# Kernel optimization log

Hardware: AMD Instinct MI355X
Metric: run time of the kernel (lower is better)

Reference implementation:

```python
import jax, jax.numpy as jnp
import numpy as np

NUM_HEADS = 6

def setup_inputs() -> dict:
    key = jax.random.key(0)
    ks = jax.random.split(key, 6)
    B_, N, C = 4096, 64, 192
    nW = 4096
    return {
        "x": jax.random.normal(ks[0], (B_, N, C), dtype=jnp.float32),
        "mask": jax.random.normal(ks[1], (nW, N, N), dtype=jnp.float32),
        "qkv_w": jax.random.normal(ks[2], (3 * C, C), dtype=jnp.float32) * 0.02,
        "qkv_b": jax.random.normal(ks[3], (3 * C,), dtype=jnp.float32) * 0.02,
        "proj_w": jax.random.normal(ks[4], (C, C), dtype=jnp.float32) * 0.02,
        "proj_b": jax.random.normal(ks[5], (C,), dtype=jnp.float32) * 0.02,
    }

def reference(x, mask, qkv_w, qkv_b, proj_w, proj_b):
    B_, N, C = x.shape
    H = NUM_HEADS
    hd = C // H
    scale = hd ** -0.5
    qkv = (x @ qkv_w.T + qkv_b).reshape(B_, N, 3, H, hd)
    qkv = jnp.transpose(qkv, (2, 0, 3, 1, 4))  # [3, B_, H, N, hd]
    q, k, v = qkv[0], qkv[1], qkv[2]
    attn = jnp.einsum('bhnd,bhmd->bhnm', q * scale, k)  # [B_, H, N, N]
    nW = mask.shape[0]
    # additive relative/shift mask broadcast over image batch and heads
    attn = attn.reshape(B_ // nW, nW, H, N, N) + mask[None, :, None, :, :]
    attn = attn.reshape(B_, H, N, N)
    attn = jax.nn.softmax(attn, axis=-1)
    out = jnp.einsum('bhnm,bhmd->bhnd', attn, v)  # [B_, H, N, hd]
    out = jnp.transpose(out, (0, 2, 1, 3)).reshape(B_, N, C)
    return out @ proj_w.T + proj_b
```

## Files before the change

### kernel.cpp

```cpp
#include <hip/hip_runtime.h>
#include <hip/hip_bf16.h>
#include <stdint.h>


#define NTOK 64
#define CDIM 192
#define KROW 40
#define VROW 72
#define CHUNK 3072

typedef __attribute__((ext_vector_type(4))) float f32x4;
typedef __attribute__((ext_vector_type(8))) short bf16x8;

__device__ __forceinline__ short f2bf(float f) {
  __hip_bfloat16 h = __float2bfloat16(f);
  return *reinterpret_cast<short*>(&h);
}
__device__ __forceinline__ uint32_t pack2(float a, float b) {
  __hip_bfloat162 h2;
  h2.x = __float2bfloat16(a);
  h2.y = __float2bfloat16(b);
  return *reinterpret_cast<uint32_t*>(&h2);
}

__device__ __forceinline__ bf16x8 xpose(uint32_t A0, uint32_t A1,
                                        uint32_t B0, uint32_t B1,
                                        int s0, int hiSel) {
  uint32_t w[4];
  uint32_t a, b;
  a = (uint32_t)__shfl((int)A0, s0);      b = (uint32_t)__shfl((int)B0, s0);      w[0] = hiSel ? b : a;
  a = (uint32_t)__shfl((int)A1, s0);      b = (uint32_t)__shfl((int)B1, s0);      w[1] = hiSel ? b : a;
  a = (uint32_t)__shfl((int)A0, s0 + 16); b = (uint32_t)__shfl((int)B0, s0 + 16); w[2] = hiSel ? b : a;
  a = (uint32_t)__shfl((int)A1, s0 + 16); b = (uint32_t)__shfl((int)B1, s0 + 16); w[3] = hiSel ? b : a;
  return *reinterpret_cast<bf16x8*>(w);
}

#define MFMA16(A, B, C) __builtin_amdgcn_mfma_f32_16x16x32_bf16((A), (B), (C), 0, 0, 0)

__device__ __forceinline__ f32x4 gemm6_w_af(const short* __restrict__ p0,
                                            const short* __restrict__ p1,
                                            const bf16x8* __restrict__ af) {
  f32x4 acc = {0.f, 0.f, 0.f, 0.f};
  acc = MFMA16(*reinterpret_cast<const bf16x8*>(p0),       af[0], acc);
  acc = MFMA16(*reinterpret_cast<const bf16x8*>(p1),       af[1], acc);
  acc = MFMA16(*reinterpret_cast<const bf16x8*>(p0 + 64),  af[2], acc);
  acc = MFMA16(*reinterpret_cast<const bf16x8*>(p1 + 64),  af[3], acc);
  acc = MFMA16(*reinterpret_cast<const bf16x8*>(p0 + 128), af[4], acc);
  acc = MFMA16(*reinterpret_cast<const bf16x8*>(p1 + 128), af[5], acc);
  return acc;
}
__device__ __forceinline__ f32x4 gemm6_af_w(const short* __restrict__ p0,
                                            const short* __restrict__ p1,
                                            const bf16x8* __restrict__ af) {
  f32x4 acc = {0.f, 0.f, 0.f, 0.f};
  acc = MFMA16(af[0], *reinterpret_cast<const bf16x8*>(p0),       acc);
  acc = MFMA16(af[1], *reinterpret_cast<const bf16x8*>(p1),       acc);
  acc = MFMA16(af[2], *reinterpret_cast<const bf16x8*>(p0 + 64),  acc);
  acc = MFMA16(af[3], *reinterpret_cast<const bf16x8*>(p1 + 64),  acc);
  acc = MFMA16(af[4], *reinterpret_cast<const bf16x8*>(p0 + 128), acc);
  acc = MFMA16(af[5], *reinterpret_cast<const bf16x8*>(p1 + 128), acc);
  return acc;
}

#define GLOAD16(g, l) __builtin_amdgcn_global_load_lds( \
    (const __attribute__((address_space(1))) void*)(g), \
    (__attribute__((address_space(3))) void*)(l), 16, 0, 0)

__global__ void wconv_kernel(const float* __restrict__ qkv_w,
                             const float* __restrict__ proj_w,
                             short* __restrict__ ws) {
  const int r = blockIdx.x, c = threadIdx.x;
  int chunk, lr;
  float val;
  if (r < 192)      { chunk = r >> 4; lr = r & 15; val = qkv_w[r * CDIM + c]; }
  else if (r < 384) { int q = r - 192; int h = q >> 5; int rr = q & 31;
                      chunk = 12 + 4 * h + (rr >> 4); lr = rr & 15; val = qkv_w[r * CDIM + c]; }
  else if (r < 576) { int q = r - 384; int h = q >> 5; int rr = q & 31;
                      chunk = 14 + 4 * h + (rr >> 4); lr = rr & 15; val = qkv_w[r * CDIM + c]; }
  else              { int q = r - 576; chunk = 36 + (q >> 4); lr = q & 15; val = proj_w[q * CDIM + c]; }
  const int s = c >> 3, lo = c & 7;
  const int sp = (s & 24) | ((s ^ lr) & 7);
  ws[chunk * CHUNK + lr * CDIM + sp * 8 + lo] = f2bf(val);
}

__global__ __launch_bounds__(256, 4)
void winattn_kernel(const float* __restrict__ x, const float* __restrict__ mask,
                    const short* __restrict__ ws,
                    const float* __restrict__ qkv_b, const float* __restrict__ proj_b,
                    float* __restrict__ out) {
  __shared__ __align__(16) short wbA[16 * CDIM];
  __shared__ __align__(16) short wbB[16 * CDIM];
  __shared__ __align__(16) short kh[NTOK * KROW];
  __shared__ __align__(16) short vth[32 * VROW];

  const int b    = blockIdx.x;
  const int tid  = threadIdx.x;
  const int lane = tid & 63;
  const int l16  = lane & 15;
  const int g4   = lane >> 4;
  const int m0   = (tid >> 6) * 16;
  const float scale = 0.17677669529663687f;
  const int s0 = (((2 * g4) & 3) << 4) + l16;
  const int hiSel = g4 >> 1;

  const int t0 = ((g4 ^ l16) & 7) << 3;
  const short* rA0 = wbA + l16 * CDIM + t0;
  const short* rA1 = wbA + l16 * CDIM + (t0 ^ 32);
  const short* rB0 = wbB + l16 * CDIM + t0;
  const short* rB1 = wbB + l16 * CDIM + (t0 ^ 32);
  const short* khr = kh + l16 * KROW + g4 * 8;
  short*       khw = kh + (m0 + l16) * KROW + 4 * g4;
  const short* vtr = vth + l16 * VROW + g4 * 8;
  short*       vtw = vth + l16 * VROW + m0 + 4 * g4;
  const int gofs = (tid >> 6) * 512 + lane * 8;
  const int lofs = (tid >> 6) * 512;
  const bool tail = (tid >> 6) < 2;

  {
    GLOAD16(ws + gofs, wbA + lofs);
    if (tail) GLOAD16(ws + gofs + 2048, wbA + lofs + 2048);
    GLOAD16(ws + CHUNK + gofs, wbB + lofs);
    if (tail) GLOAD16(ws + CHUNK + gofs + 2048, wbB + lofs + 2048);
  }
  const float* xr = x + (size_t)b * (NTOK * CDIM) + (m0 + l16) * CDIM;
  bf16x8 af[6];
  #pragma unroll
  for (int ks = 0; ks < 6; ++ks) {
    const float4 v0 = *reinterpret_cast<const float4*>(xr + ks * 32 + g4 * 8);
    const float4 v1 = *reinterpret_cast<const float4*>(xr + ks * 32 + g4 * 8 + 4);
    uint32_t t[4];
    t[0] = pack2(v0.x, v0.y); t[1] = pack2(v0.z, v0.w);
    t[2] = pack2(v1.x, v1.y); t[3] = pack2(v1.z, v1.w);
    af[ks] = *reinterpret_cast<bf16x8*>(t);
  }
  const float* mrowl = mask + (size_t)b * (NTOK * NTOK) + (m0 + l16) * NTOK;

  __syncthreads();

#define STAGE(dst, cidx) do { \
    GLOAD16(ws + (cidx) * CHUNK + gofs, (dst) + lofs); \
    if (tail) GLOAD16(ws + (cidx) * CHUNK + gofs + 2048, (dst) + lofs + 2048); \
  } while (0)

  bf16x8 aq[6];
  uint32_t ue0 = 0, ue1 = 0;
  #pragma unroll
  for (int c = 0; c < 12; ++c) {
    const bool odd = (c & 1);
    f32x4 acc = odd ? gemm6_w_af(rB0, rB1, af) : gemm6_w_af(rA0, rA1, af);
    const float4 bq = *reinterpret_cast<const float4*>(qkv_b + 16 * c + 4 * g4);
    const uint32_t u0 = pack2((acc[0] + bq.x) * scale, (acc[1] + bq.y) * scale);
    const uint32_t u1 = pack2((acc[2] + bq.z) * scale, (acc[3] + bq.w) * scale);
    if (odd) aq[c >> 1] = xpose(ue0, ue1, u0, u1, s0, hiSel);
    else     { ue0 = u0; ue1 = u1; }
    __syncthreads();
    STAGE(odd ? wbB : wbA, c + 2);
  }

  bf16x8 of[6];
  bf16x8 bpa, bpb;
  #pragma unroll
  for (int h = 0; h < 6; ++h) {
    const int base = 12 + 4 * h;
    {
      f32x4 acc = gemm6_w_af(rA0, rA1, af);
      const float4 bk4 = *reinterpret_cast<const float4*>(qkv_b + 192 + 32 * h + 4 * g4);
      uint2 kw;
      kw.x = pack2(acc[0] + bk4.x, acc[1] + bk4.y);
      kw.y = pack2(acc[2] + bk4.z, acc[3] + bk4.w);
      *reinterpret_cast<uint2*>(khw) = kw;
    }
    if (h > 0) {
      uint32_t uo[2][2];
      #pragma unroll
      for (int ct2 = 0; ct2 < 2; ++ct2) {
        const short* vb = vtr + ct2 * (16 * VROW);
        f32x4 acc = {0.f, 0.f, 0.f, 0.f};
        acc = MFMA16(*reinterpret_cast<const bf16x8*>(vb),      bpa, acc);
        acc = MFMA16(*reinterpret_cast<const bf16x8*>(vb + 32), bpb, acc);
        uo[ct2][0] = pack2(acc[0], acc[1]);
        uo[ct2][1] = pack2(acc[2], acc[3]);
      }
      of[h - 1] = xpose(uo[0][0], uo[0][1], uo[1][0], uo[1][1], s0, hiSel);
    }
    __syncthreads();
    STAGE(wbA, base + 2);

    {
      f32x4 acc = gemm6_w_af(rB0, rB1, af);
      const float4 bk4 = *reinterpret_cast<const float4*>(qkv_b + 192 + 32 * h + 16 + 4 * g4);
      uint2 kw;
      kw.x = pack2(acc[0] + bk4.x, acc[1] + bk4.y);
      kw.y = pack2(acc[2] + bk4.z, acc[3] + bk4.w);
      *reinterpret_cast<uint2*>(khw + 16) = kw;
    }
    __syncthreads();
    STAGE(wbB, base + 3);

    {
      f32x4 acc = gemm6_af_w(rA0, rA1, af);
      const float bv = qkv_b[384 + 32 * h + l16];
      uint2 vw;
      vw.x = pack2(acc[0] + bv, acc[1] + bv);
      vw.y = pack2(acc[2] + bv, acc[3] + bv);
      *reinterpret_cast<uint2*>(vtw) = vw;
    }
    {
      float pr[4][4];
      float rmax = -1e30f;
      #pragma unroll
      for (int rt = 0; rt < 4; ++rt) {
        f32x4 z = {0.f, 0.f, 0.f, 0.f};
        f32x4 s = MFMA16(*reinterpret_cast<const bf16x8*>(khr + rt * (16 * KROW)), aq[h], z);
        const float4 mv = *reinterpret_cast<const float4*>(mrowl + 16 * rt + 4 * g4);
        pr[rt][0] = s[0] + mv.x; pr[rt][1] = s[1] + mv.y;
        pr[rt][2] = s[2] + mv.z; pr[rt][3] = s[3] + mv.w;
        #pragma unroll
        for (int i = 0; i < 4; ++i) rmax = fmaxf(rmax, pr[rt][i]);
      }
      rmax = fmaxf(rmax, __shfl_xor(rmax, 16));
      rmax = fmaxf(rmax, __shfl_xor(rmax, 32));
      float rsum = 0.f;
      #pragma unroll
      for (int rt = 0; rt < 4; ++rt)
        #pragma unroll
        for (int i = 0; i < 4; ++i) { pr[rt][i] = __expf(pr[rt][i] - rmax); rsum += pr[rt][i]; }
      rsum += __shfl_xor(rsum, 16);
      rsum += __shfl_xor(rsum, 32);
      const float rinv = 1.f / rsum;
      uint32_t wpk[4][2];
      #pragma unroll
      for (int rt = 0; rt < 4; ++rt) {
        wpk[rt][0] = pack2(pr[rt][0] * rinv, pr[rt][1] * rinv);
        wpk[rt][1] = pack2(pr[rt][2] * rinv, pr[rt][3] * rinv);
      }
      bpa = xpose(wpk[0][0], wpk[0][1], wpk[1][0], wpk[1][1], s0, hiSel);
      bpb = xpose(wpk[2][0], wpk[2][1], wpk[3][0], wpk[3][1], s0, hiSel);
    }
    __syncthreads();
    STAGE(wbA, h < 5 ? base + 4 : 36);

    {
      f32x4 acc = gemm6_af_w(rB0, rB1, af);
      const float bv = qkv_b[384 + 32 * h + 16 + l16];
      uint2 vw;
      vw.x = pack2(acc[0] + bv, acc[1] + bv);
      vw.y = pack2(acc[2] + bv, acc[3] + bv);
      *reinterpret_cast<uint2*>(vtw + 16 * VROW) = vw;
    }
    __syncthreads();
    STAGE(wbB, h < 5 ? base + 5 : 37);
  }

  float* og = out + (size_t)b * (NTOK * CDIM);
  #pragma unroll
  for (int j = 0; j < 12; ++j) {
    const bool odd = (j & 1);
    if (j == 0) {
      uint32_t uo[2][2];
      #pragma unroll
      for (int ct2 = 0; ct2 < 2; ++ct2) {
        const short* vb = vtr + ct2 * (16 * VROW);
        f32x4 acc = {0.f, 0.f, 0.f, 0.f};
        acc = MFMA16(*reinterpret_cast<const bf16x8*>(vb),      bpa, acc);
        acc = MFMA16(*reinterpret_cast<const bf16x8*>(vb + 32), bpb, acc);
        uo[ct2][0] = pack2(acc[0], acc[1]);
        uo[ct2][1] = pack2(acc[2], acc[3]);
      }
      of[5] = xpose(uo[0][0], uo[0][1], uo[1][0], uo[1][1], s0, hiSel);
    }
    f32x4 acc = odd ? gemm6_af_w(rB0, rB1, of) : gemm6_af_w(rA0, rA1, of);
    const int cc = 16 * j + l16;
    const float pb = proj_b[cc];
    #pragma unroll
    for (int i = 0; i < 4; ++i)
      og[(m0 + 4 * g4 + i) * CDIM + cc] = acc[i] + pb;
    if (j < 10) {
      __syncthreads();
      STAGE(odd ? wbB : wbA, 38 + j);
    } else if (j == 10) {
      __syncthreads();
    }
  }
#undef STAGE
}

extern "C" void kernel_launch(void* const* d_in, const int* in_sizes, int n_in,
                              void* d_out, int out_size, void* d_ws, size_t ws_size,
                              hipStream_t stream) {
  const float* x      = (const float*)d_in[0];
  const float* mask   = (const float*)d_in[1];
  const float* qkv_w  = (const float*)d_in[2];
  const float* qkv_b  = (const float*)d_in[3];
  const float* proj_w = (const float*)d_in[4];
  const float* proj_b = (const float*)d_in[5];
  float* out = (float*)d_out;

  short* ws = (short*)d_ws;

  wconv_kernel<<<768, 192, 0, stream>>>(qkv_w, proj_w, ws);
  winattn_kernel<<<4096, 256, 0, stream>>>(x, mask, ws, qkv_b, proj_b, out);
}
```

Measured before the change: 207.3 us.

## Interleave per-head Q projection into head loop to cut registers, raise occupancy

Moves the Q projection from a separate upfront pass (which kept all six heads' Q fragments live in registers) into the per-head loop, and reorders the weight chunks so each head's Q, K and V chunks are contiguous. This shrinks register pressure by holding only one head's Q fragment at a time. Launch bounds are raised from 4 to 5 blocks per SIMD to use the freed registers for occupancy. The risk is spills if the compiler cannot fit the tighter register budget.

```diff
diff --git a/kernel.cpp b/kernel.cpp
--- a/kernel.cpp
+++ b/kernel.cpp
@@ -72,18 +72,20 @@
   const int r = blockIdx.x, c = threadIdx.x;
   int chunk, lr;
   float val;
-  if (r < 192)      { chunk = r >> 4; lr = r & 15; val = qkv_w[r * CDIM + c]; }
-  else if (r < 384) { int q = r - 192; int h = q >> 5; int rr = q & 31;
-                      chunk = 12 + 4 * h + (rr >> 4); lr = rr & 15; val = qkv_w[r * CDIM + c]; }
-  else if (r < 576) { int q = r - 384; int h = q >> 5; int rr = q & 31;
-                      chunk = 14 + 4 * h + (rr >> 4); lr = rr & 15; val = qkv_w[r * CDIM + c]; }
-  else              { int q = r - 576; chunk = 36 + (q >> 4); lr = q & 15; val = proj_w[q * CDIM + c]; }
+  if (r < 192)      { int h = r >> 5; chunk = 6 * h + ((r >> 4) & 1); lr = r & 15;
+                      val = qkv_w[r * CDIM + c]; }
+  else if (r < 384) { int q = r - 192; int h = q >> 5; chunk = 6 * h + 2 + ((q >> 4) & 1);
+                      lr = q & 15; val = qkv_w[r * CDIM + c]; }
+  else if (r < 576) { int q = r - 384; int h = q >> 5; chunk = 6 * h + 4 + ((q >> 4) & 1);
+                      lr = q & 15; val = qkv_w[r * CDIM + c]; }
+  else              { int q = r - 576; chunk = 36 + (q >> 4); lr = q & 15;
+                      val = proj_w[q * CDIM + c]; }
   const int s = c >> 3, lo = c & 7;
   const int sp = (s & 24) | ((s ^ lr) & 7);
   ws[chunk * CHUNK + lr * CDIM + sp * 8 + lo] = f2bf(val);
 }
 
-__global__ __launch_bounds__(256, 4)
+__global__ __launch_bounds__(256, 5)
 void winattn_kernel(const float* __restrict__ x, const float* __restrict__ mask,
                     const short* __restrict__ ws,
                     const float* __restrict__ qkv_b, const float* __restrict__ proj_b,
@@ -142,33 +144,17 @@
     if (tail) GLOAD16(ws + (cidx) * CHUNK + gofs + 2048, (dst) + lofs + 2048); \
   } while (0)
 
-  bf16x8 aq[6];
-  uint32_t ue0 = 0, ue1 = 0;
-  #pragma unroll
-  for (int c = 0; c < 12; ++c) {
-    const bool odd = (c & 1);
-    f32x4 acc = odd ? gemm6_w_af(rB0, rB1, af) : gemm6_w_af(rA0, rA1, af);
-    const float4 bq = *reinterpret_cast<const float4*>(qkv_b + 16 * c + 4 * g4);
-    const uint32_t u0 = pack2((acc[0] + bq.x) * scale, (acc[1] + bq.y) * scale);
-    const uint32_t u1 = pack2((acc[2] + bq.z) * scale, (acc[3] + bq.w) * scale);
-    if (odd) aq[c >> 1] = xpose(ue0, ue1, u0, u1, s0, hiSel);
-    else     { ue0 = u0; ue1 = u1; }
-    __syncthreads();
-    STAGE(odd ? wbB : wbA, c + 2);
-  }
-
   bf16x8 of[6];
   bf16x8 bpa, bpb;
   #pragma unroll
   for (int h = 0; h < 6; ++h) {
-    const int base = 12 + 4 * h;
+    const int base = 6 * h;
+    uint32_t ue0, ue1;
     {
       f32x4 acc = gemm6_w_af(rA0, rA1, af);
-      const float4 bk4 = *reinterpret_cast<const float4*>(qkv_b + 192 + 32 * h + 4 * g4);
-      uint2 kw;
-      kw.x = pack2(acc[0] + bk4.x, acc[1] + bk4.y);
-      kw.y = pack2(acc[2] + bk4.z, acc[3] + bk4.w);
-      *reinterpret_cast<uint2*>(khw) = kw;
+      const float4 bq = *reinterpret_cast<const float4*>(qkv_b + 32 * h + 4 * g4);
+      ue0 = pack2((acc[0] + bq.x) * scale, (acc[1] + bq.y) * scale);
+      ue1 = pack2((acc[2] + bq.z) * scale, (acc[3] + bq.w) * scale);
     }
     if (h > 0) {
       uint32_t uo[2][2];
@@ -186,6 +172,28 @@
     __syncthreads();
     STAGE(wbA, base + 2);
 
+    bf16x8 aqh;
+    {
+      f32x4 acc = gemm6_w_af(rB0, rB1, af);
+      const float4 bq = *reinterpret_cast<const float4*>(qkv_b + 32 * h + 16 + 4 * g4);
+      const uint32_t u0 = pack2((acc[0] + bq.x) * scale, (acc[1] + bq.y) * scale);
+      const uint32_t u1 = pack2((acc[2] + bq.z) * scale, (acc[3] + bq.w) * scale);
+      aqh = xpose(ue0, ue1, u0, u1, s0, hiSel);
+    }
+    __syncthreads();
+    STAGE(wbB, base + 3);
+
+    {
+      f32x4 acc = gemm6_w_af(rA0, rA1, af);
+      const float4 bk4 = *reinterpret_cast<const float4*>(qkv_b + 192 + 32 * h + 4 * g4);
+      uint2 kw;
+      kw.x = pack2(acc[0] + bk4.x, acc[1] + bk4.y);
+      kw.y = pack2(acc[2] + bk4.z, acc[3] + bk4.w);
+      *reinterpret_cast<uint2*>(khw) = kw;
+    }
+    __syncthreads();
+    STAGE(wbA, base + 4);
+
     {
       f32x4 acc = gemm6_w_af(rB0, rB1, af);
       const float4 bk4 = *reinterpret_cast<const float4*>(qkv_b + 192 + 32 * h + 16 + 4 * g4);
@@ -195,7 +203,7 @@
       *reinterpret_cast<uint2*>(khw + 16) = kw;
     }
     __syncthreads();
-    STAGE(wbB, base + 3);
+    STAGE(wbB, base + 5);
 
     {
       f32x4 acc = gemm6_af_w(rA0, rA1, af);
@@ -211,7 +219,7 @@
       #pragma unroll
       for (int rt = 0; rt < 4; ++rt) {
         f32x4 z = {0.f, 0.f, 0.f, 0.f};
-        f32x4 s = MFMA16(*reinterpret_cast<const bf16x8*>(khr + rt * (16 * KROW)), aq[h], z);
+        f32x4 s = MFMA16(*reinterpret_cast<const bf16x8*>(khr + rt * (16 * KROW)), aqh, z);
         const float4 mv = *reinterpret_cast<const float4*>(mrowl + 16 * rt + 4 * g4);
         pr[rt][0] = s[0] + mv.x; pr[rt][1] = s[1] + mv.y;
         pr[rt][2] = s[2] + mv.z; pr[rt][3] = s[3] + mv.w;
@@ -238,7 +246,7 @@
       bpb = xpose(wpk[2][0], wpk[2][1], wpk[3][0], wpk[3][1], s0, hiSel);
     }
     __syncthreads();
-    STAGE(wbA, h < 5 ? base + 4 : 36);
+    STAGE(wbA, h < 5 ? base + 6 : 36);
 
     {
       f32x4 acc = gemm6_af_w(rB0, rB1, af);
@@ -249,7 +257,7 @@
       *reinterpret_cast<uint2*>(vtw + 16 * VROW) = vw;
     }
     __syncthreads();
-    STAGE(wbB, h < 5 ? base + 5 : 37);
+    STAGE(wbB, h < 5 ? base + 7 : 37);
   }
 
   float* og = out + (size_t)b * (NTOK * CDIM);
```

After: 223.3 us. +7.7%, slower.
